# Kernel tuning notes

Measured on AMD Instinct MI355X. Metric: run time of the kernel, lower is better.

## Reference

```python
import jax, jax.numpy as jnp
import numpy as np

N_STATE = 1024
N_HEAD = 16


def setup_inputs() -> dict:
    key = jax.random.key(0)
    ks = jax.random.split(key, 8)
    B, C, H, W = 4, N_STATE, 1, 1500
    s = C ** -0.5
    return {
        "x": jax.random.normal(ks[0], (B, C, H, W), dtype=jnp.float32),
        "Wq": jax.random.normal(ks[1], (C, C), dtype=jnp.float32) * s,
        "bq": jnp.zeros((C,), dtype=jnp.float32),
        "Wk": jax.random.normal(ks[2], (C, C), dtype=jnp.float32) * s,
        "Wv": jax.random.normal(ks[3], (C, C), dtype=jnp.float32) * s,
        "bv": jnp.zeros((C,), dtype=jnp.float32),
        "Wo": jax.random.normal(ks[4], (C, C), dtype=jnp.float32) * s,
        "bo": jnp.zeros((C,), dtype=jnp.float32),
    }


def reference(x, Wq, bq, Wk, Wv, bv, Wo, bo):
    B, C, H, W = x.shape
    nh = N_HEAD
    d = C // nh
    scale = d ** -0.5

    def conv1x1(w, b=None):
        y = jnp.einsum('bchw,oc->bohw', x, w)  # 1x1 conv == per-pixel matmul
        return y if b is None else y + b[None, :, None, None]

    # [B, nh, d, H, W] per-head layout (channel split matches torch .split)
    q = conv1x1(Wq, bq).reshape(B, nh, d, H, W)
    k = conv1x1(Wk).reshape(B, nh, d, H, W)
    v = conv1x1(Wv, bv).reshape(B, nh, d, H, W)

    # attention along width axis, independently per height row and head
    scores = jnp.einsum('bndhq,bndhk->bnhqk', q, k) * scale  # [B,nh,H,Wq,Wk]
    attn = jax.nn.softmax(scores, axis=-1)                   # softmax over keys
    o = jnp.einsum('bnhqk,bndhk->bndhq', attn, v).reshape(B, C, H, W)
    return jnp.einsum('bchw,oc->bohw', o, Wo) + bo[None, :, None, None]
```

## Files before the change

kernel.cpp:

```cpp
#include <hip/hip_runtime.h>
#include <stdint.h>


typedef unsigned short u16;
typedef __bf16 bf16x8 __attribute__((ext_vector_type(8)));
typedef __bf16 bf16x4 __attribute__((ext_vector_type(4)));
typedef float  f32x4  __attribute__((ext_vector_type(4)));
typedef unsigned int __attribute__((address_space(1))) as1_uint;
typedef unsigned int __attribute__((address_space(3))) as3_uint;

__device__ __forceinline__ u16 f2bf(float f) {
    unsigned u = __float_as_uint(f);
    u += 0x7fffu + ((u >> 16) & 1u);
    return (u16)(u >> 16);
}

__device__ __forceinline__ f32x4 fzero4() { f32x4 z = {0.f, 0.f, 0.f, 0.f}; return z; }

__device__ __forceinline__ void gld16(void* lds, const void* g) {
    __builtin_amdgcn_global_load_lds((const as1_uint*)g, (as3_uint*)lds, 16, 0, 0);
}

__global__ void wconv_k(const float* __restrict__ wq, const float* __restrict__ wk,
                        const float* __restrict__ wv, const float* __restrict__ wo,
                        u16* __restrict__ wb) {
    unsigned idx = blockIdx.x * 256u + threadIdx.x;
    unsigned m = idx >> 18, r = idx & 0x3ffffu;
    const float* s = (m == 0) ? wq : (m == 1) ? wk : (m == 2) ? wv : wo;
    float4 v = ((const float4*)s)[r];
    uint2 o;
    o.x = (unsigned)f2bf(v.x) | ((unsigned)f2bf(v.y) << 16);
    o.y = (unsigned)f2bf(v.z) | ((unsigned)f2bf(v.w) << 16);
    ((uint2*)(wb + (m << 20)))[r] = o;
}

__global__ void xpose_k(const float* __restrict__ x, u16* __restrict__ xb) {
    __shared__ float tile[64][65];
    const int b = blockIdx.z;
    const int w0 = blockIdx.x * 64, c0 = blockIdx.y * 64;
    const int tw = threadIdx.x & 63, t4 = threadIdx.x >> 6;
#pragma unroll
    for (int i = 0; i < 16; i++) {
        int c = i * 4 + t4;
        int w = w0 + tw;
        tile[c][tw] = (w < 1500) ? x[((b << 10) + c0 + c) * 1500 + w] : 0.f;
    }
    __syncthreads();
#pragma unroll
    for (int i = 0; i < 16; i++) {
        int wl = i * 4 + t4;
        int w = w0 + wl;
        if (w < 1500) xb[((b * 1500 + w) << 10) + c0 + tw] = f2bf(tile[tw][wl]);
    }
}

__device__ __forceinline__ void gemm_core(const u16* __restrict__ A, int arow0, int amax,
                                          const u16* __restrict__ Bm, int brow0, int bmax,
                                          f32x4 (&acc)[4][4], unsigned char* lds) {
    const int t = threadIdx.x, l15 = t & 15, lg = (t >> 4) & 3;
    const int wv = t >> 6, wm = wv >> 1, wn = wv & 1;
#pragma unroll
    for (int im = 0; im < 4; im++)
#pragma unroll
        for (int in = 0; in < 4; in++) acc[im][in] = fzero4();

    for (int kt = 0; kt < 32; kt++) {
        const int k0 = kt << 5;
        __syncthreads();
#pragma unroll
        for (int i = 0; i < 2; i++) {
            int xo = (i * 256 + t) << 4;
            int row = xo >> 6, seg = (xo >> 4) & 3;
            int ar = arow0 + row; if (ar > amax) ar = amax;
            int br = brow0 + row; if (br > bmax) br = bmax;
            gld16(lds + xo,        A  + ((long)ar << 10) + k0 + seg * 8);
            gld16(lds + 8192 + xo, Bm + ((long)br << 10) + k0 + seg * 8);
        }
        __syncthreads();
        bf16x8 af[4], bfr[4];
#pragma unroll
        for (int im = 0; im < 4; im++)
            af[im] = *(const bf16x8*)(lds + ((wm * 64 + im * 16 + l15) << 6) + (lg << 4));
#pragma unroll
        for (int in = 0; in < 4; in++)
            bfr[in] = *(const bf16x8*)(lds + 8192 + ((wn * 64 + in * 16 + l15) << 6) + (lg << 4));
#pragma unroll
        for (int im = 0; im < 4; im++)
#pragma unroll
            for (int in = 0; in < 4; in++)
                acc[im][in] = __builtin_amdgcn_mfma_f32_16x16x32_bf16(af[im], bfr[in], acc[im][in], 0, 0, 0);
    }
}

__global__ __launch_bounds__(256) void gemm_qk_k(const u16* __restrict__ xb, const u16* __restrict__ wb,
                                                 const float* __restrict__ bq,
                                                 u16* __restrict__ Q, u16* __restrict__ K) {
    __shared__ __attribute__((aligned(16))) unsigned char lds[16384];
    const int z = blockIdx.z;
    f32x4 acc[4][4];
    gemm_core(xb, blockIdx.x * 128, 5999, wb + (z << 20), blockIdx.y * 128, 1023, acc, lds);

    const int t = threadIdx.x, l15 = t & 15, lg = (t >> 4) & 3;
    const int wv = t >> 6, wm = wv >> 1, wn = wv & 1;
    const int m0 = blockIdx.x * 128 + wm * 64;
    const int n0 = blockIdx.y * 128 + wn * 64;
    u16* dst = z ? K : Q;
    const float* bias = z ? nullptr : bq;
#pragma unroll
    for (int im = 0; im < 4; im++) {
#pragma unroll
        for (int r = 0; r < 4; r++) {
            int tok = m0 + im * 16 + lg * 4 + r;
            if (tok < 6000) {
                int b = tok / 1500, w = tok - b * 1500;
#pragma unroll
                for (int in = 0; in < 4; in++) {
                    int o = n0 + in * 16 + l15;
                    float v = acc[im][in][r] + (bias ? bias[o] : 0.f);
                    dst[((((b << 4) + (o >> 6)) * 1500 + w) << 6) + (o & 63)] = f2bf(v);
                }
            }
        }
    }
}

__global__ __launch_bounds__(256) void gemm_v_k(const u16* __restrict__ xb, const u16* __restrict__ wb,
                                                const float* __restrict__ bv, u16* __restrict__ Vt) {
    __shared__ __attribute__((aligned(16))) unsigned char lds[16384];
    const int b = blockIdx.z;
    f32x4 acc[4][4];
    gemm_core(wb + (2u << 20), blockIdx.x * 128, 1023, xb + b * 1500 * 1024, blockIdx.y * 128, 1499, acc, lds);
    const int t = threadIdx.x, l15 = t & 15, lg = (t >> 4) & 3;
    const int wv = t >> 6, wm = wv >> 1, wn = wv & 1;
    const int m0 = blockIdx.x * 128 + wm * 64;
    const int n0 = blockIdx.y * 128 + wn * 64;
#pragma unroll
    for (int im = 0; im < 4; im++) {
#pragma unroll
        for (int r = 0; r < 4; r++) {
            int o = m0 + im * 16 + lg * 4 + r;
            float bi = bv[o];
#pragma unroll
            for (int in = 0; in < 4; in++) {
                int w = n0 + in * 16 + l15;
                if (w < 1500)      Vt[((b << 10) + o) * 1504 + w] = f2bf(acc[im][in][r] + bi);
                else if (w < 1504) Vt[((b << 10) + o) * 1504 + w] = 0;
            }
        }
    }
}

__global__ __launch_bounds__(256) void gemm_out_k(const u16* __restrict__ Ow, const u16* __restrict__ wb,
                                                  const float* __restrict__ bo, float* __restrict__ out) {
    __shared__ __attribute__((aligned(16))) unsigned char lds[16384];
    const int b = blockIdx.z;
    f32x4 acc[4][4];
    gemm_core(wb + (3u << 20), blockIdx.x * 128, 1023, Ow + b * 1500 * 1024, blockIdx.y * 128, 1499, acc, lds);
    const int t = threadIdx.x, l15 = t & 15, lg = (t >> 4) & 3;
    const int wv = t >> 6, wm = wv >> 1, wn = wv & 1;
    const int m0 = blockIdx.x * 128 + wm * 64;
    const int n0 = blockIdx.y * 128 + wn * 64;
#pragma unroll
    for (int im = 0; im < 4; im++) {
#pragma unroll
        for (int r = 0; r < 4; r++) {
            int o = m0 + im * 16 + lg * 4 + r;
            float bi = bo[o];
#pragma unroll
            for (int in = 0; in < 4; in++) {
                int w = n0 + in * 16 + l15;
                if (w < 1500) out[(long)((b << 10) + o) * 1500 + w] = acc[im][in][r] + bi;
            }
        }
    }
}

__global__ __launch_bounds__(512) void attn_k(const u16* __restrict__ Q, const u16* __restrict__ K,
                                              const u16* __restrict__ Vt, u16* __restrict__ O) {
    __shared__ __attribute__((aligned(16))) unsigned char lds[51200];

    const int qt = blockIdx.x, bh = blockIdx.y;
    const int b = bh >> 4, h = bh & 15;
    const int t = threadIdx.x, wv = t >> 6, l15 = t & 15, g = (t >> 4) & 3;
    const int sk7 = l15 & 7;
    unsigned char* Pw = lds + 32768 + wv * 2304;

    int q_a = qt * 128 + wv * 16 + l15; if (q_a > 1499) q_a = 1499;
    const u16* qrow = Q + (((long)bh * 1500 + q_a) << 6);
    bf16x8 qb0 = *(const bf16x8*)(qrow + (g << 3));
    bf16x8 qb1 = *(const bf16x8*)(qrow + 32 + (g << 3));

    const u16* Kbh = K + (((long)bh * 1500) << 6);
    const u16* Vtb = Vt + (long)((b << 10) + (h << 6)) * 1504;

    const int srow = t >> 3;
    const int ssw  = ((t & 7) ^ (srow & 7)) << 3;
    unsigned char* kdst = lds + (t << 4);
    unsigned char* vdst = lds + 16384 + (t << 4);

    f32x4 o_acc[4];
#pragma unroll
    for (int nf = 0; nf < 4; nf++) o_acc[nf] = fzero4();
    float m_run = -1e30f, l_part = 0.f;
    const float SC = 0.18033688011112042f;

    {
        int kg = srow;
        gld16(kdst, Kbh + ((long)kg << 6) + ssw);
        gld16(vdst, Vtb + (long)srow * 1504 + ssw);
    }
    __syncthreads();

    for (int tile = 0; tile < 24; ++tile) {
        const int cur = tile & 1;
        if (tile < 23) {
            int kv0 = (tile + 1) << 6;
            int kg = kv0 + srow; if (kg > 1499) kg = 1499;
            gld16(kdst + ((cur ^ 1) << 13), Kbh + ((long)kg << 6) + ssw);
            int vc = kv0 + ssw; if (vc > 1496) vc = 1496;
            gld16(vdst + ((cur ^ 1) << 13), Vtb + (long)srow * 1504 + vc);
        }
        const unsigned char* Kl = lds + (cur << 13);
        const unsigned char* Vl = lds + 16384 + (cur << 13);

        f32x4 s[4];
#pragma unroll
        for (int kt = 0; kt < 4; kt++) {
            const unsigned char* kp = Kl + ((kt * 16 + l15) << 7);
            bf16x8 ka0 = *(const bf16x8*)(kp + ((g ^ sk7) << 4));
            bf16x8 ka1 = *(const bf16x8*)(kp + (((g + 4) ^ sk7) << 4));
            f32x4 z = fzero4();
            z = __builtin_amdgcn_mfma_f32_16x16x32_bf16(ka0, qb0, z, 0, 0, 0);
            z = __builtin_amdgcn_mfma_f32_16x16x32_bf16(ka1, qb1, z, 0, 0, 0);
            s[kt] = z;
        }
        if (tile == 23) {
#pragma unroll
            for (int kt = 0; kt < 4; kt++)
#pragma unroll
                for (int r = 0; r < 4; r++)
                    if (kt * 16 + g * 4 + r >= 28) s[kt][r] = -1e30f;
        }

        float mx = fmaxf(fmaxf(fmaxf(s[0][0], s[0][1]), fmaxf(s[0][2], s[0][3])),
                         fmaxf(fmaxf(s[1][0], s[1][1]), fmaxf(s[1][2], s[1][3])));
        float mx2 = fmaxf(fmaxf(fmaxf(s[2][0], s[2][1]), fmaxf(s[2][2], s[2][3])),
                          fmaxf(fmaxf(s[3][0], s[3][1]), fmaxf(s[3][2], s[3][3])));
        mx = fmaxf(mx, mx2);
        mx = fmaxf(mx, __shfl_xor(mx, 16));
        mx = fmaxf(mx, __shfl_xor(mx, 32));

        if (!__all(mx <= m_run + 44.f)) {
            float mnew = fmaxf(m_run, mx);
            float sc = exp2f((m_run - mnew) * SC);
            l_part *= sc;
#pragma unroll
            for (int r = 0; r < 4; r++) {
                float sco = __shfl(sc, g * 4 + r);
#pragma unroll
                for (int nf = 0; nf < 4; nf++) o_acc[nf][r] *= sco;
            }
            m_run = mnew;
        }

        const float msc = m_run * SC;
        float psum = 0.f;
#pragma unroll
        for (int kt = 0; kt < 4; kt++) {
            float p0 = exp2f(fmaf(s[kt][0], SC, -msc));
            float p1 = exp2f(fmaf(s[kt][1], SC, -msc));
            float p2 = exp2f(fmaf(s[kt][2], SC, -msc));
            float p3 = exp2f(fmaf(s[kt][3], SC, -msc));
            psum += (p0 + p1) + (p2 + p3);
            bf16x4 pk;
            pk[0] = (__bf16)p0; pk[1] = (__bf16)p1; pk[2] = (__bf16)p2; pk[3] = (__bf16)p3;
            *(bf16x4*)(Pw + l15 * 144 + kt * 32 + g * 8) = pk;
        }
        l_part += psum;

#pragma unroll
        for (int hh = 0; hh < 2; hh++) {
            bf16x8 pa = *(const bf16x8*)(Pw + l15 * 144 + hh * 64 + g * 16);
#pragma unroll
            for (int nf = 0; nf < 4; nf++) {
                const unsigned char* vp = Vl + ((nf * 16 + l15) << 7);
                bf16x8 vb = *(const bf16x8*)(vp + (((g + 4 * hh) ^ sk7) << 4));
                o_acc[nf] = __builtin_amdgcn_mfma_f32_16x16x32_bf16(pa, vb, o_acc[nf], 0, 0, 0);
            }
        }
        __syncthreads();
    }

    l_part += __shfl_xor(l_part, 16);
    l_part += __shfl_xor(l_part, 32);
    float inv = 1.f / l_part;
#pragma unroll
    for (int r = 0; r < 4; r++) {
        float invr = __shfl(inv, g * 4 + r);
        int q = qt * 128 + wv * 16 + g * 4 + r;
        if (q < 1500) {
            u16* dst = O + ((long)(b * 1500 + q) << 10) + (h << 6);
#pragma unroll
            for (int nf = 0; nf < 4; nf++)
                dst[nf * 16 + l15] = f2bf(o_acc[nf][r] * invr);
        }
    }
}

extern "C" void kernel_launch(void* const* d_in, const int* in_sizes, int n_in,
                              void* d_out, int out_size, void* d_ws, size_t ws_size,
                              hipStream_t stream) {
    const float* x  = (const float*)d_in[0];
    const float* Wq = (const float*)d_in[1];
    const float* bq = (const float*)d_in[2];
    const float* Wk = (const float*)d_in[3];
    const float* Wv = (const float*)d_in[4];
    const float* bv = (const float*)d_in[5];
    const float* Wo = (const float*)d_in[6];
    const float* bo = (const float*)d_in[7];
    float* out = (float*)d_out;

    const size_t NEED = 57573376;
    if (ws_size < NEED) return;

    unsigned char* ws = (unsigned char*)d_ws;
    u16* xb = (u16*)(ws);
    u16* wb = (u16*)(ws + 12288000);
    u16* Qw = (u16*)(ws + 20676608);
    u16* Kw = (u16*)(ws + 32964608);
    u16* Vt = (u16*)(ws + 45252608);

    wconv_k<<<dim3(4096), dim3(256), 0, stream>>>(Wq, Wk, Wv, Wo, wb);
    xpose_k<<<dim3(24, 16, 4), dim3(256), 0, stream>>>(x, xb);
    gemm_qk_k<<<dim3(47, 8, 2), dim3(256), 0, stream>>>(xb, wb, bq, Qw, Kw);
    gemm_v_k<<<dim3(8, 12, 4), dim3(256), 0, stream>>>(xb, wb, bv, Vt);
    attn_k<<<dim3(12, 64), dim3(512), 0, stream>>>(Qw, Kw, Vt, xb );
    gemm_out_k<<<dim3(8, 12, 4), dim3(256), 0, stream>>>(xb, wb, bo, out);
}
```

Before: 196.4 us.

## Fuse prep and QKV kernels, widen GEMM K-tile with swizzle, keep P in registers

Merges the weight conversion and x transpose into one launch, and the QK and V projections into one launch. The GEMM core now uses 64-wide K tiles with an XOR-swizzled LDS layout to cut bank conflicts and halve the number of barriers. In attention, V is stored with permuted columns so the probability tile can feed the PV MFMA straight from registers instead of going through LDS, and s_setprio is raised around the MFMA sections. The larger LDS footprint in the GEMMs may lower occupancy, and the permuted V layout must exactly match the register fragment order.

```diff
diff --git a/kernel.cpp b/kernel.cpp
--- a/kernel.cpp
+++ b/kernel.cpp
@@ -4,7 +4,6 @@
 
 typedef unsigned short u16;
 typedef __bf16 bf16x8 __attribute__((ext_vector_type(8)));
-typedef __bf16 bf16x4 __attribute__((ext_vector_type(4)));
 typedef float  f32x4  __attribute__((ext_vector_type(4)));
 typedef unsigned int __attribute__((address_space(1))) as1_uint;
 typedef unsigned int __attribute__((address_space(3))) as3_uint;
@@ -21,145 +20,159 @@
     __builtin_amdgcn_global_load_lds((const as1_uint*)g, (as3_uint*)lds, 16, 0, 0);
 }
 
-__global__ void wconv_k(const float* __restrict__ wq, const float* __restrict__ wk,
-                        const float* __restrict__ wv, const float* __restrict__ wo,
-                        u16* __restrict__ wb) {
-    unsigned idx = blockIdx.x * 256u + threadIdx.x;
-    unsigned m = idx >> 18, r = idx & 0x3ffffu;
-    const float* s = (m == 0) ? wq : (m == 1) ? wk : (m == 2) ? wv : wo;
-    float4 v = ((const float4*)s)[r];
-    uint2 o;
-    o.x = (unsigned)f2bf(v.x) | ((unsigned)f2bf(v.y) << 16);
-    o.y = (unsigned)f2bf(v.z) | ((unsigned)f2bf(v.w) << 16);
-    ((uint2*)(wb + (m << 20)))[r] = o;
-}
-
-__global__ void xpose_k(const float* __restrict__ x, u16* __restrict__ xb) {
+__device__ __forceinline__ int permw(int w) {
+    return (w & ~31) | ((w & 12) << 1) | ((w & 16) >> 2) | (w & 3);
+}
+
+__global__ void prep_k(const float* __restrict__ wq, const float* __restrict__ wk,
+                       const float* __restrict__ wv, const float* __restrict__ wo,
+                       u16* __restrict__ wb, const float* __restrict__ x,
+                       u16* __restrict__ xb) {
     __shared__ float tile[64][65];
-    const int b = blockIdx.z;
-    const int w0 = blockIdx.x * 64, c0 = blockIdx.y * 64;
-    const int tw = threadIdx.x & 63, t4 = threadIdx.x >> 6;
-#pragma unroll
-    for (int i = 0; i < 16; i++) {
-        int c = i * 4 + t4;
-        int w = w0 + tw;
-        tile[c][tw] = (w < 1500) ? x[((b << 10) + c0 + c) * 1500 + w] : 0.f;
-    }
-    __syncthreads();
-#pragma unroll
-    for (int i = 0; i < 16; i++) {
-        int wl = i * 4 + t4;
-        int w = w0 + wl;
-        if (w < 1500) xb[((b * 1500 + w) << 10) + c0 + tw] = f2bf(tile[tw][wl]);
-    }
-}
-
-__device__ __forceinline__ void gemm_core(const u16* __restrict__ A, int arow0, int amax,
-                                          const u16* __restrict__ Bm, int brow0, int bmax,
-                                          f32x4 (&acc)[4][4], unsigned char* lds) {
+    const int bid = blockIdx.x;
+    if (bid < 4096) {
+        unsigned idx = bid * 256u + threadIdx.x;
+        unsigned m = idx >> 18, r = idx & 0x3ffffu;
+        const float* s = (m == 0) ? wq : (m == 1) ? wk : (m == 2) ? wv : wo;
+        float4 v = ((const float4*)s)[r];
+        uint2 o;
+        o.x = (unsigned)f2bf(v.x) | ((unsigned)f2bf(v.y) << 16);
+        o.y = (unsigned)f2bf(v.z) | ((unsigned)f2bf(v.w) << 16);
+        ((uint2*)(wb + (m << 20)))[r] = o;
+    } else {
+        int bid2 = bid - 4096;
+        const int xw = bid2 % 24, yc = (bid2 / 24) & 15, b = bid2 / 384;
+        const int w0 = xw * 64, c0 = yc * 64;
+        const int tw = threadIdx.x & 63, t4 = threadIdx.x >> 6;
+#pragma unroll
+        for (int i = 0; i < 16; i++) {
+            int c = i * 4 + t4, w = w0 + tw;
+            tile[c][tw] = (w < 1500) ? x[((b << 10) + c0 + c) * 1500 + w] : 0.f;
+        }
+        __syncthreads();
+#pragma unroll
+        for (int i = 0; i < 16; i++) {
+            int wl = i * 4 + t4, w = w0 + wl;
+            if (w < 1500) xb[((b * 1500 + w) << 10) + c0 + tw] = f2bf(tile[tw][wl]);
+        }
+    }
+}
+
+__device__ __forceinline__ void gemm_core64(const u16* __restrict__ A, int arow0, int amax,
+                                            const u16* __restrict__ Bm, int brow0, int bmax,
+                                            f32x4 (&acc)[4][4], unsigned char* lds) {
     const int t = threadIdx.x, l15 = t & 15, lg = (t >> 4) & 3;
     const int wv = t >> 6, wm = wv >> 1, wn = wv & 1;
+    const int l7 = l15 & 7;
 #pragma unroll
     for (int im = 0; im < 4; im++)
 #pragma unroll
         for (int in = 0; in < 4; in++) acc[im][in] = fzero4();
 
-    for (int kt = 0; kt < 32; kt++) {
-        const int k0 = kt << 5;
+    for (int kt = 0; kt < 16; kt++) {
+        const int k0 = kt << 6;
         __syncthreads();
 #pragma unroll
-        for (int i = 0; i < 2; i++) {
+        for (int i = 0; i < 4; i++) {
             int xo = (i * 256 + t) << 4;
-            int row = xo >> 6, seg = (xo >> 4) & 3;
+            int row = xo >> 7, seg = (xo >> 4) & 7;
+            int sseg = seg ^ (row & 7);
             int ar = arow0 + row; if (ar > amax) ar = amax;
             int br = brow0 + row; if (br > bmax) br = bmax;
-            gld16(lds + xo,        A  + ((long)ar << 10) + k0 + seg * 8);
-            gld16(lds + 8192 + xo, Bm + ((long)br << 10) + k0 + seg * 8);
+            gld16(lds + xo,         A  + ((long)ar << 10) + k0 + sseg * 8);
+            gld16(lds + 16384 + xo, Bm + ((long)br << 10) + k0 + sseg * 8);
         }
         __syncthreads();
-        bf16x8 af[4], bfr[4];
-#pragma unroll
-        for (int im = 0; im < 4; im++)
-            af[im] = *(const bf16x8*)(lds + ((wm * 64 + im * 16 + l15) << 6) + (lg << 4));
-#pragma unroll
-        for (int in = 0; in < 4; in++)
-            bfr[in] = *(const bf16x8*)(lds + 8192 + ((wn * 64 + in * 16 + l15) << 6) + (lg << 4));
-#pragma unroll
-        for (int im = 0; im < 4; im++)
-#pragma unroll
-            for (int in = 0; in < 4; in++)
-                acc[im][in] = __builtin_amdgcn_mfma_f32_16x16x32_bf16(af[im], bfr[in], acc[im][in], 0, 0, 0);
-    }
-}
-
-__global__ __launch_bounds__(256) void gemm_qk_k(const u16* __restrict__ xb, const u16* __restrict__ wb,
-                                                 const float* __restrict__ bq,
-                                                 u16* __restrict__ Q, u16* __restrict__ K) {
-    __shared__ __attribute__((aligned(16))) unsigned char lds[16384];
-    const int z = blockIdx.z;
+#pragma unroll
+        for (int ks = 0; ks < 2; ks++) {
+            bf16x8 af[4], bfr[4];
+#pragma unroll
+            for (int im = 0; im < 4; im++) {
+                int row = wm * 64 + im * 16 + l15;
+                af[im] = *(const bf16x8*)(lds + (row << 7) + (((ks * 4 + lg) ^ l7) << 4));
+            }
+#pragma unroll
+            for (int in = 0; in < 4; in++) {
+                int row = wn * 64 + in * 16 + l15;
+                bfr[in] = *(const bf16x8*)(lds + 16384 + (row << 7) + (((ks * 4 + lg) ^ l7) << 4));
+            }
+#pragma unroll
+            for (int im = 0; im < 4; im++)
+#pragma unroll
+                for (int in = 0; in < 4; in++)
+                    acc[im][in] = __builtin_amdgcn_mfma_f32_16x16x32_bf16(af[im], bfr[in], acc[im][in], 0, 0, 0);
+        }
+    }
+}
+
+__global__ __launch_bounds__(256) void qkv_k(const u16* __restrict__ xb, const u16* __restrict__ wb,
+                                             const float* __restrict__ bq, const float* __restrict__ bv,
+                                             u16* __restrict__ Q, u16* __restrict__ K,
+                                             u16* __restrict__ Vt) {
+    __shared__ __attribute__((aligned(16))) unsigned char lds[32768];
+    const int bid = blockIdx.x;
+    const int t = threadIdx.x, l15 = t & 15, lg = (t >> 4) & 3;
+    const int wv = t >> 6, wm = wv >> 1, wn = wv & 1;
     f32x4 acc[4][4];
-    gemm_core(xb, blockIdx.x * 128, 5999, wb + (z << 20), blockIdx.y * 128, 1023, acc, lds);
-
+
+    if (bid < 752) {
+        const int z = bid / 376, rem = bid % 376;
+        const int xt = rem % 47, yt = rem / 47;
+        gemm_core64(xb, xt * 128, 5999, wb + (z << 20), yt * 128, 1023, acc, lds);
+        const int m0 = xt * 128 + wm * 64, n0 = yt * 128 + wn * 64;
+        u16* dst = z ? K : Q;
+        const float* bias = z ? nullptr : bq;
+#pragma unroll
+        for (int im = 0; im < 4; im++) {
+#pragma unroll
+            for (int r = 0; r < 4; r++) {
+                int tok = m0 + im * 16 + lg * 4 + r;
+                if (tok < 6000) {
+                    int b = tok / 1500, w = tok - b * 1500;
+#pragma unroll
+                    for (int in = 0; in < 4; in++) {
+                        int o = n0 + in * 16 + l15;
+                        float v = acc[im][in][r] + (bias ? bias[o] : 0.f);
+                        dst[((((b << 4) + (o >> 6)) * 1500 + w) << 6) + (o & 63)] = f2bf(v);
+                    }
+                }
+            }
+        }
+    } else {
+        const int rem = bid - 752;
+        const int xt = rem & 7, rest = rem >> 3;
+        const int yt = rest % 12, b = rest / 12;
+        gemm_core64(wb + (2u << 20), xt * 128, 1023, xb + b * 1500 * 1024, yt * 128, 1499, acc, lds);
+        const int m0 = xt * 128 + wm * 64, n0 = yt * 128 + wn * 64;
+#pragma unroll
+        for (int im = 0; im < 4; im++) {
+#pragma unroll
+            for (int r = 0; r < 4; r++) {
+                int o = m0 + im * 16 + lg * 4 + r;
+                float bi = bv[o];
+#pragma unroll
+                for (int in = 0; in < 4; in++) {
+                    int w = n0 + in * 16 + l15;
+                    if (w < 1504) {
+                        u16 val = (w < 1500) ? f2bf(acc[im][in][r] + bi) : (u16)0;
+                        Vt[((b << 10) + o) * 1504 + permw(w)] = val;
+                    }
+                }
+            }
+        }
+    }
+}
+
+__global__ __launch_bounds__(256) void gemm_out_k(const u16* __restrict__ Ow, const u16* __restrict__ wb,
+                                                  const float* __restrict__ bo, float* __restrict__ out) {
+    __shared__ __attribute__((aligned(16))) unsigned char lds[32768];
+    const int b = blockIdx.z;
+    f32x4 acc[4][4];
+    gemm_core64(wb + (3u << 20), blockIdx.x * 128, 1023, Ow + b * 1500 * 1024, blockIdx.y * 128, 1499, acc, lds);
     const int t = threadIdx.x, l15 = t & 15, lg = (t >> 4) & 3;
     const int wv = t >> 6, wm = wv >> 1, wn = wv & 1;
     const int m0 = blockIdx.x * 128 + wm * 64;
     const int n0 = blockIdx.y * 128 + wn * 64;
-    u16* dst = z ? K : Q;
-    const float* bias = z ? nullptr : bq;
-#pragma unroll
-    for (int im = 0; im < 4; im++) {
-#pragma unroll
-        for (int r = 0; r < 4; r++) {
-            int tok = m0 + im * 16 + lg * 4 + r;
-            if (tok < 6000) {
-                int b = tok / 1500, w = tok - b * 1500;
-#pragma unroll
-                for (int in = 0; in < 4; in++) {
-                    int o = n0 + in * 16 + l15;
-                    float v = acc[im][in][r] + (bias ? bias[o] : 0.f);
-                    dst[((((b << 4) + (o >> 6)) * 1500 + w) << 6) + (o & 63)] = f2bf(v);
-                }
-            }
-        }
-    }
-}
-
-__global__ __launch_bounds__(256) void gemm_v_k(const u16* __restrict__ xb, const u16* __restrict__ wb,
-                                                const float* __restrict__ bv, u16* __restrict__ Vt) {
-    __shared__ __attribute__((aligned(16))) unsigned char lds[16384];
-    const int b = blockIdx.z;
-    f32x4 acc[4][4];
-    gemm_core(wb + (2u << 20), blockIdx.x * 128, 1023, xb + b * 1500 * 1024, blockIdx.y * 128, 1499, acc, lds);
-    const int t = threadIdx.x, l15 = t & 15, lg = (t >> 4) & 3;
-    const int wv = t >> 6, wm = wv >> 1, wn = wv & 1;
-    const int m0 = blockIdx.x * 128 + wm * 64;
-    const int n0 = blockIdx.y * 128 + wn * 64;
-#pragma unroll
-    for (int im = 0; im < 4; im++) {
-#pragma unroll
-        for (int r = 0; r < 4; r++) {
-            int o = m0 + im * 16 + lg * 4 + r;
-            float bi = bv[o];
-#pragma unroll
-            for (int in = 0; in < 4; in++) {
-                int w = n0 + in * 16 + l15;
-                if (w < 1500)      Vt[((b << 10) + o) * 1504 + w] = f2bf(acc[im][in][r] + bi);
-                else if (w < 1504) Vt[((b << 10) + o) * 1504 + w] = 0;
-            }
-        }
-    }
-}
-
-__global__ __launch_bounds__(256) void gemm_out_k(const u16* __restrict__ Ow, const u16* __restrict__ wb,
-                                                  const float* __restrict__ bo, float* __restrict__ out) {
-    __shared__ __attribute__((aligned(16))) unsigned char lds[16384];
-    const int b = blockIdx.z;
-    f32x4 acc[4][4];
-    gemm_core(wb + (3u << 20), blockIdx.x * 128, 1023, Ow + b * 1500 * 1024, blockIdx.y * 128, 1499, acc, lds);
-    const int t = threadIdx.x, l15 = t & 15, lg = (t >> 4) & 3;
-    const int wv = t >> 6, wm = wv >> 1, wn = wv & 1;
-    const int m0 = blockIdx.x * 128 + wm * 64;
-    const int n0 = blockIdx.y * 128 + wn * 64;
 #pragma unroll
     for (int im = 0; im < 4; im++) {
 #pragma unroll
@@ -177,13 +190,12 @@
 
 __global__ __launch_bounds__(512) void attn_k(const u16* __restrict__ Q, const u16* __restrict__ K,
                                               const u16* __restrict__ Vt, u16* __restrict__ O) {
-    __shared__ __attribute__((aligned(16))) unsigned char lds[51200];
+    __shared__ __attribute__((aligned(16))) unsigned char lds[32768];
 
     const int qt = blockIdx.x, bh = blockIdx.y;
     const int b = bh >> 4, h = bh & 15;
     const int t = threadIdx.x, wv = t >> 6, l15 = t & 15, g = (t >> 4) & 3;
     const int sk7 = l15 & 7;
-    unsigned char* Pw = lds + 32768 + wv * 2304;
 
     int q_a = qt * 128 + wv * 16 + l15; if (q_a > 1499) q_a = 1499;
     const u16* qrow = Q + (((long)bh * 1500 + q_a) << 6);
@@ -204,11 +216,8 @@
     float m_run = -1e30f, l_part = 0.f;
     const float SC = 0.18033688011112042f;
 
-    {
-        int kg = srow;
-        gld16(kdst, Kbh + ((long)kg << 6) + ssw);
-        gld16(vdst, Vtb + (long)srow * 1504 + ssw);
-    }
+    gld16(kdst, Kbh + ((long)srow << 6) + ssw);
+    gld16(vdst, Vtb + (long)srow * 1504 + ssw);
     __syncthreads();
 
     for (int tile = 0; tile < 24; ++tile) {
@@ -224,6 +233,7 @@
         const unsigned char* Vl = lds + 16384 + (cur << 13);
 
         f32x4 s[4];
+        __builtin_amdgcn_s_setprio(1);
 #pragma unroll
         for (int kt = 0; kt < 4; kt++) {
             const unsigned char* kp = Kl + ((kt * 16 + l15) << 7);
@@ -234,6 +244,7 @@
             z = __builtin_amdgcn_mfma_f32_16x16x32_bf16(ka1, qb1, z, 0, 0, 0);
             s[kt] = z;
         }
+        __builtin_amdgcn_s_setprio(0);
         if (tile == 23) {
 #pragma unroll
             for (int kt = 0; kt < 4; kt++)
@@ -242,11 +253,12 @@
                     if (kt * 16 + g * 4 + r >= 28) s[kt][r] = -1e30f;
         }
 
-        float mx = fmaxf(fmaxf(fmaxf(s[0][0], s[0][1]), fmaxf(s[0][2], s[0][3])),
-                         fmaxf(fmaxf(s[1][0], s[1][1]), fmaxf(s[1][2], s[1][3])));
-        float mx2 = fmaxf(fmaxf(fmaxf(s[2][0], s[2][1]), fmaxf(s[2][2], s[2][3])),
-                          fmaxf(fmaxf(s[3][0], s[3][1]), fmaxf(s[3][2], s[3][3])));
-        mx = fmaxf(mx, mx2);
+        float m1 = fmaxf(fmaxf(s[0][0], s[0][1]), s[0][2]);
+        float m2 = fmaxf(fmaxf(s[0][3], s[1][0]), s[1][1]);
+        float m3 = fmaxf(fmaxf(s[1][2], s[1][3]), s[2][0]);
+        float m4 = fmaxf(fmaxf(s[2][1], s[2][2]), s[2][3]);
+        float m5 = fmaxf(fmaxf(s[3][0], s[3][1]), s[3][2]);
+        float mx = fmaxf(fmaxf(fmaxf(m1, m2), m3), fmaxf(fmaxf(m4, m5), s[3][3]));
         mx = fmaxf(mx, __shfl_xor(mx, 16));
         mx = fmaxf(mx, __shfl_xor(mx, 32));
 
@@ -264,30 +276,36 @@
         }
 
         const float msc = m_run * SC;
+        float pv[4][4];
         float psum = 0.f;
 #pragma unroll
         for (int kt = 0; kt < 4; kt++) {
-            float p0 = exp2f(fmaf(s[kt][0], SC, -msc));
-            float p1 = exp2f(fmaf(s[kt][1], SC, -msc));
-            float p2 = exp2f(fmaf(s[kt][2], SC, -msc));
-            float p3 = exp2f(fmaf(s[kt][3], SC, -msc));
-            psum += (p0 + p1) + (p2 + p3);
-            bf16x4 pk;
-            pk[0] = (__bf16)p0; pk[1] = (__bf16)p1; pk[2] = (__bf16)p2; pk[3] = (__bf16)p3;
-            *(bf16x4*)(Pw + l15 * 144 + kt * 32 + g * 8) = pk;
+#pragma unroll
+            for (int r = 0; r < 4; r++) {
+                float p = exp2f(fmaf(s[kt][r], SC, -msc));
+                pv[kt][r] = p;
+                psum += p;
+            }
         }
         l_part += psum;
 
-#pragma unroll
-        for (int hh = 0; hh < 2; hh++) {
-            bf16x8 pa = *(const bf16x8*)(Pw + l15 * 144 + hh * 64 + g * 16);
-#pragma unroll
-            for (int nf = 0; nf < 4; nf++) {
-                const unsigned char* vp = Vl + ((nf * 16 + l15) << 7);
-                bf16x8 vb = *(const bf16x8*)(vp + (((g + 4 * hh) ^ sk7) << 4));
-                o_acc[nf] = __builtin_amdgcn_mfma_f32_16x16x32_bf16(pa, vb, o_acc[nf], 0, 0, 0);
-            }
-        }
+        bf16x8 pa0, pa1;
+#pragma unroll
+        for (int j = 0; j < 8; j++) {
+            pa0[j] = (__bf16)pv[j >> 2][j & 3];
+            pa1[j] = (__bf16)pv[2 + (j >> 2)][j & 3];
+        }
+
+        __builtin_amdgcn_s_setprio(1);
+#pragma unroll
+        for (int nf = 0; nf < 4; nf++) {
+            const unsigned char* vp = Vl + ((nf * 16 + l15) << 7);
+            bf16x8 vb0 = *(const bf16x8*)(vp + ((g ^ sk7) << 4));
+            bf16x8 vb1 = *(const bf16x8*)(vp + (((4 + g) ^ sk7) << 4));
+            o_acc[nf] = __builtin_amdgcn_mfma_f32_16x16x32_bf16(pa0, vb0, o_acc[nf], 0, 0, 0);
+            o_acc[nf] = __builtin_amdgcn_mfma_f32_16x16x32_bf16(pa1, vb1, o_acc[nf], 0, 0, 0);
+        }
+        __builtin_amdgcn_s_setprio(0);
         __syncthreads();
     }
 
@@ -330,10 +348,8 @@
     u16* Kw = (u16*)(ws + 32964608);
     u16* Vt = (u16*)(ws + 45252608);
 
-    wconv_k<<<dim3(4096), dim3(256), 0, stream>>>(Wq, Wk, Wv, Wo, wb);
-    xpose_k<<<dim3(24, 16, 4), dim3(256), 0, stream>>>(x, xb);
-    gemm_qk_k<<<dim3(47, 8, 2), dim3(256), 0, stream>>>(xb, wb, bq, Qw, Kw);
-    gemm_v_k<<<dim3(8, 12, 4), dim3(256), 0, stream>>>(xb, wb, bv, Vt);
+    prep_k<<<dim3(5632), dim3(256), 0, stream>>>(Wq, Wk, Wv, Wo, wb, x, xb);
+    qkv_k<<<dim3(1136), dim3(256), 0, stream>>>(xb, wb, bq, bv, Qw, Kw, Vt);
     attn_k<<<dim3(12, 64), dim3(512), 0, stream>>>(Qw, Kw, Vt, xb );
     gemm_out_k<<<dim3(8, 12, 4), dim3(256), 0, stream>>>(xb, wb, bo, out);
 }
```

Measured after the change: 197.7 us. No clear change (+0.7%).
